# Kernel tuning notes

Measured on AMD Instinct MI355X. Metric: run time of the kernel, lower is better.

Reference implementation:

```python
import jax, jax.numpy as jnp
import numpy as np

N = 50000          # nodes per node type
E = 1_600_000      # edges per canonical etype (avg degree 32)
IN_F = 385         # BERT_EMBEDDING_DIM(384) + NUMERICAL_FEATURES(1)
H = 128            # HIDDEN_DIM
# ntype order: 0=Policy, 1=Control, 2=ComplianceRequirement, 3=Risk
# etypes (src_ntype, dst_ntype): implements, mitigates, violates, addresses, informs
ETYPES = [(0, 1), (1, 3), (3, 2), (0, 2), (2, 0)]


def setup_inputs() -> dict:
    key = jax.random.key(0)
    ks = jax.random.split(key, 12)
    inp = {}
    names = ["feat_policy", "feat_control", "feat_compliance", "feat_risk"]
    for i, n in enumerate(names):
        inp[n] = jax.random.normal(ks[i], (N, IN_F), jnp.float32)
    inp["src"] = jax.random.randint(ks[4], (5, E), 0, N, jnp.int32)
    inp["dst"] = jax.random.randint(ks[5], (5, E), 0, N, jnp.int32)
    s_in = 1.0 / np.sqrt(IN_F).astype(np.float32)
    s_h = np.sqrt(6.0 / (H + H)).astype(np.float32)  # xavier_uniform for GraphConv
    inp["Wp"] = jax.random.uniform(ks[6], (4, IN_F, H), jnp.float32, -s_in, s_in)
    inp["bp"] = jax.random.uniform(ks[7], (4, H), jnp.float32, -s_in, s_in)
    inp["Wc1"] = jax.random.uniform(ks[8], (5, H, H), jnp.float32, -s_h, s_h)
    inp["bc1"] = jnp.zeros((5, H), jnp.float32)
    inp["Wc2"] = jax.random.uniform(ks[9], (5, H, H), jnp.float32, -s_h, s_h)
    inp["bc2"] = jnp.zeros((5, H), jnp.float32)
    return inp


def _graph_conv(x, s, d, W, b):
    """DGL GraphConv(norm='both'): D_dst^{-1/2} A D_src^{-1/2} X W + b."""
    ones = jnp.ones(s.shape[0], x.dtype)
    deg_out = jnp.clip(jax.ops.segment_sum(ones, s, num_segments=N), 1.0)
    deg_in = jnp.clip(jax.ops.segment_sum(ones, d, num_segments=N), 1.0)
    xs = x * jax.lax.rsqrt(deg_out)[:, None]            # [N, H] scale by src out-deg
    agg = jax.ops.segment_sum(xs[s], d, num_segments=N)  # gather + scatter-sum [N, H]
    agg = agg * jax.lax.rsqrt(deg_in)[:, None]
    return agg @ W + b


def reference(feat_policy, feat_control, feat_compliance, feat_risk,
              src, dst, Wp, bp, Wc1, bc1, Wc2, bc2):
    feats = [feat_policy, feat_control, feat_compliance, feat_risk]
    # input projections + relu per node type
    h = [jax.nn.relu(f @ Wp[i] + bp[i]) for i, f in enumerate(feats)]

    def hetero_layer(h, Wc, bc):
        out = [jnp.zeros((N, H), h[0].dtype) for _ in range(4)]
        for k, (st, dt) in enumerate(ETYPES):  # HeteroGraphConv aggregate='sum'
            out[dt] = out[dt] + _graph_conv(h[st], src[k], dst[k], Wc[k], bc[k])
        return out

    h = [jax.nn.relu(v) for v in hetero_layer(h, Wc1, bc1)]
    h = [jax.nn.relu(v) for v in hetero_layer(h, Wc2, bc2)]
    return jnp.stack(h)  # [4, N, H] final embeddings per node type
```

## Files before the change

kernel.cpp:

```cpp
#include <hip/hip_runtime.h>
#include <hip/hip_bf16.h>

#define INF 385
#define HD 128
#define NWG 16

typedef __attribute__((ext_vector_type(8))) short short8;
typedef __attribute__((ext_vector_type(4))) float f32x4;

__device__ inline unsigned short f2b(float f) {
    __hip_bfloat16 h = __float2bfloat16(f);
    return *reinterpret_cast<unsigned short*>(&h);
}
__device__ inline float b2f(unsigned int lo16) {
    union { unsigned int u; float f; } c; c.u = lo16 << 16; return c.f;
}

__global__ __launch_bounds__(1024) void hist_kernel(
    const int* __restrict__ src_all, const int* __restrict__ dst_all,
    unsigned short* __restrict__ partial,
    unsigned short* __restrict__ rank_local,
    int E, int N)
{
    __shared__ unsigned int cnt[25000];
    int g = blockIdx.x / NWG;
    int w = blockIdx.x % NWG;
    int tid = threadIdx.x;
    int half = (N + 1) / 2;
    for (int i = tid; i < half; i += 1024) cnt[i] = 0;
    __syncthreads();

    int C = (E + NWG - 1) / NWG;
    int lo = w * C, hi = min(lo + C, E);
    if (g < 5) {
        const int* arr = dst_all + (size_t)g * E;
        for (int e = lo + tid; e < hi; e += 1024) {
            int d = __builtin_nontemporal_load(&arr[e]);
            unsigned int sh = (d & 1) * 16;
            unsigned int old = atomicAdd(&cnt[d >> 1], 1u << sh);
            rank_local[(size_t)g * E + e] = (unsigned short)((old >> sh) & 0xffffu);
        }
    } else {
        const int* arr = src_all + (size_t)(g - 5) * E;
        for (int e = lo + tid; e < hi; e += 1024) {
            int d = __builtin_nontemporal_load(&arr[e]);
            atomicAdd(&cnt[d >> 1], 1u << ((d & 1) * 16));
        }
    }
    __syncthreads();
    unsigned short* outp = partial + ((size_t)g * NWG + w) * N;
    for (int n = tid; n < N; n += 1024)
        outp[n] = (unsigned short)((cnt[n >> 1] >> ((n & 1) * 16)) & 0xffffu);
}

__global__ void reduce_kernel(unsigned short* __restrict__ partial, int* __restrict__ cnt_dst,
                              float* __restrict__ rsq_out, float* __restrict__ rsq_in, int N) {
    int i = blockIdx.x * blockDim.x + threadIdx.x;
    int stride = gridDim.x * blockDim.x;
    int tot = 10 * N;
    for (; i < tot; i += stride) {
        int g = i / N, n = i - g * N;
        unsigned short* p = partial + ((size_t)g * NWG) * N + n;
        int sum = 0;
        #pragma unroll
        for (int w = 0; w < NWG; ++w) {
            int v = p[(size_t)w * N];
            p[(size_t)w * N] = (unsigned short)sum;
            sum += v;
        }
        float r = rsqrtf((float)max(sum, 1));
        if (g < 5) { cnt_dst[i] = sum; rsq_in[i] = r; }
        else rsq_out[i - 5 * N] = r;
    }
}

__global__ __launch_bounds__(1024) void scan_kernel(const int* __restrict__ cnt_all,
                                                    int* __restrict__ off_all, int n) {
    const int* cnt = cnt_all + (size_t)blockIdx.x * n;
    int* off = off_all + (size_t)blockIdx.x * (n + 1);
    __shared__ int ssum[1024];
    int t = threadIdx.x;
    int chunk = (n + 1023) / 1024;
    int lo = t * chunk, hi = min(lo + chunk, n);
    int s = 0;
    for (int i = lo; i < hi; ++i) s += cnt[i];
    ssum[t] = s;
    __syncthreads();
    for (int d = 1; d < 1024; d <<= 1) {
        int v = (t >= d) ? ssum[t - d] : 0;
        __syncthreads();
        ssum[t] += v;
        __syncthreads();
    }
    int excl = (t == 0) ? 0 : ssum[t - 1];
    for (int i = lo; i < hi; ++i) { off[i] = excl; excl += cnt[i]; }
    if (t == 1023) off[n] = ssum[1023];
}

__global__ void permute_kernel(const int* __restrict__ src_all, const int* __restrict__ dst_all,
                               const int* __restrict__ off, const unsigned short* __restrict__ partial,
                               const unsigned short* __restrict__ rank_local,
                               unsigned short* __restrict__ sorted, int E, int N) {
    int i = blockIdx.x * blockDim.x + threadIdx.x;
    int stride = gridDim.x * blockDim.x;
    int tot = 5 * E;
    int C = (E + NWG - 1) / NWG;
    for (; i < tot; i += stride) {
        int k = i / E, e = i - k * E;
        int w = e / C;
        int d = __builtin_nontemporal_load(&dst_all[i]);
        int s = __builtin_nontemporal_load(&src_all[i]);
        int rl = __builtin_nontemporal_load(&rank_local[i]);
        int pos = off[(size_t)k * (N + 1) + d]
                + partial[((size_t)k * NWG + w) * N + d]
                + rl;
        __builtin_nontemporal_store((unsigned short)s, &sorted[(size_t)k * E + pos]);
    }
}

__global__ void convert_kernel(const float* __restrict__ f0, const float* __restrict__ f1,
                               const float* __restrict__ f2, const float* __restrict__ f3,
                               unsigned int* __restrict__ featB,
                               float* __restrict__ alast, int N) {
    int i = blockIdx.x * blockDim.x + threadIdx.x;
    int stride = gridDim.x * blockDim.x;
    int per = N * 192;
    int tot = 4 * per;
    for (int p = i; p < tot; p += stride) {
        int t = p / per, rem = p - t * per;
        int n = rem / 192, c2 = (rem - n * 192) * 2;
        const float* f = (t < 2) ? (t == 0 ? f0 : f1) : (t == 2 ? f2 : f3);
        const float* row = f + (size_t)n * INF;
        float a = row[c2], b = row[c2 + 1];
        featB[p] = ((unsigned int)f2b(b) << 16) | f2b(a);
    }
    for (int p = i; p < 4 * N; p += stride) {
        int t = p / N, n = p - t * N;
        const float* f = (t < 2) ? (t == 0 ? f0 : f1) : (t == 2 ? f2 : f3);
        alast[p] = f[(size_t)n * INF + 384];
    }
}

__global__ void prep_weights_kernel(const float* __restrict__ Wp,
                                    const float* __restrict__ Wc1, const float* __restrict__ Wc2,
                                    const float* __restrict__ bc1, const float* __restrict__ bc2,
                                    unsigned short* __restrict__ WpT,
                                    unsigned short* __restrict__ WcT,
                                    float* __restrict__ cbias) {
    int i = blockIdx.x * blockDim.x + threadIdx.x;
    int stride = gridDim.x * blockDim.x;
    const int nWp = 4 * 128 * 384;
    for (int p = i; p < nWp; p += stride) {
        int t = p / (128 * 384), rem = p % (128 * 384);
        int c = rem / 384, k = rem % 384;
        WpT[p] = f2b(Wp[(size_t)t * INF * HD + (size_t)k * HD + c]);
    }
    const int nWc = 5 * 128 * 128;
    for (int p = i; p < 2 * nWc; p += stride) {
        int layer = p / nWc, rem = p % nWc;
        int e = rem / (128 * 128), rem2 = rem % (128 * 128);
        int c = rem2 / 128, k = rem2 % 128;
        const float* W = layer ? Wc2 : Wc1;
        WcT[p] = f2b(W[(size_t)e * 128 * 128 + (size_t)k * 128 + c]);
    }
    for (int p = i; p < 2 * 4 * 128; p += stride) {
        int layer = p / 512, rem = p % 512;
        int t = rem / 128, c = rem % 128;
        const float* bc = layer ? bc2 : bc1;
        float v;
        if (t == 0) v = bc[4 * 128 + c];
        else if (t == 1) v = bc[0 * 128 + c];
        else if (t == 2) v = bc[2 * 128 + c] + bc[3 * 128 + c];
        else v = bc[1 * 128 + c];
        cbias[p] = v;
    }
}

struct GemmDesc {
    const unsigned short* A;
    const unsigned short* Bt;
    const float* bias;
    const float* rowscale;
    const float* alast;
    const float* wlast;
    unsigned short* out;
};
struct GemmBatch { GemmDesc d[5]; };

__global__ __launch_bounds__(256) void gemm_mfma_kernel(
    GemmBatch batch, int lda, int M, int K, int relu)
{
    const GemmDesc dsc = batch.d[blockIdx.y];
    const unsigned short* __restrict__ Bt = dsc.Bt;
    const unsigned short* __restrict__ A = dsc.A;

    __shared__ __align__(16) unsigned short As[64][72];
    __shared__ __align__(16) unsigned short Bs[128][72];
    const int tid = threadIdx.x;
    const int bm = blockIdx.x * 64;
    const int wid = tid >> 6, lane = tid & 63;
    const int wr = wid & 1, wc = wid >> 1;
    const int l15 = lane & 15, l4 = lane >> 4;

    f32x4 acc[2][4] = {};

    for (int k0 = 0; k0 < K; k0 += 64) {
        {
            int r = tid >> 2, q = tid & 3;
            int gm = bm + r;
            if (gm < M) {
                const uint4* g = (const uint4*)(A + (size_t)gm * lda + k0 + q * 16);
                *(uint4*)&As[r][q * 16] = g[0];
                *(uint4*)&As[r][q * 16 + 8] = g[1];
            } else {
                uint4 z = {0, 0, 0, 0};
                *(uint4*)&As[r][q * 16] = z;
                *(uint4*)&As[r][q * 16 + 8] = z;
            }
        }
        {
            int col = tid >> 1, hf = tid & 1;
            const uint4* g = (const uint4*)(Bt + (size_t)col * K + k0 + hf * 32);
            #pragma unroll
            for (int j = 0; j < 4; ++j)
                *(uint4*)&Bs[col][hf * 32 + j * 8] = g[j];
        }
        __syncthreads();
        #pragma unroll
        for (int kk = 0; kk < 2; ++kk) {
            short8 a[2], b[4];
            #pragma unroll
            for (int mi = 0; mi < 2; ++mi)
                a[mi] = *(const short8*)&As[wr * 32 + mi * 16 + l15][kk * 32 + l4 * 8];
            #pragma unroll
            for (int ni = 0; ni < 4; ++ni)
                b[ni] = *(const short8*)&Bs[wc * 64 + ni * 16 + l15][kk * 32 + l4 * 8];
            #pragma unroll
            for (int mi = 0; mi < 2; ++mi)
                #pragma unroll
                for (int ni = 0; ni < 4; ++ni)
                    acc[mi][ni] = __builtin_amdgcn_mfma_f32_16x16x32_bf16(
                        a[mi], b[ni], acc[mi][ni], 0, 0, 0);
        }
        __syncthreads();
    }

    #pragma unroll
    for (int mi = 0; mi < 2; ++mi) {
        #pragma unroll
        for (int r = 0; r < 4; ++r) {
            int grow = bm + wr * 32 + mi * 16 + l4 * 4 + r;
            if (grow >= M) continue;
            float rs = dsc.rowscale ? dsc.rowscale[grow] : 1.f;
            float al = dsc.alast ? dsc.alast[grow] : 0.f;
            #pragma unroll
            for (int ni = 0; ni < 4; ++ni) {
                int gcol = wc * 64 + ni * 16 + l15;
                float v = acc[mi][ni][r];
                if (dsc.wlast) v += al * dsc.wlast[gcol];
                if (dsc.bias) v += dsc.bias[gcol];
                v *= rs;
                if (relu) v = fmaxf(v, 0.f);
                dsc.out[(size_t)grow * HD + gcol] = f2b(v);
            }
        }
    }
}

struct GatherDesc {
    const unsigned short* msgA; const unsigned short* sortedA;
    const int* offA; const float* rsqA;
    const unsigned short* msgB; const unsigned short* sortedB;
    const int* offB; const float* rsqB;
    const float* bias; void* out;
};
struct GatherBatch { GatherDesc d[4]; };

template<int OUT_BF16>
__global__ __launch_bounds__(256) void gather_kernel(GatherBatch batch, int n)
{
    const GatherDesc d = batch.d[blockIdx.y];
    int node = blockIdx.x * 4 + (threadIdx.x >> 6);
    if (node >= n) return;
    int lane = threadIdx.x & 63;

    float ox, oy;
    {
        float ax = 0.f, ay = 0.f;
        int beg = d.offA[node], end = d.offA[node + 1];
        int e = beg;
        for (; e + 3 < end; e += 4) {
            int s0 = d.sortedA[e], s1 = d.sortedA[e + 1];
            int s2 = d.sortedA[e + 2], s3 = d.sortedA[e + 3];
            unsigned int v0 = *(const unsigned int*)(d.msgA + (size_t)s0 * HD + lane * 2);
            unsigned int v1 = *(const unsigned int*)(d.msgA + (size_t)s1 * HD + lane * 2);
            unsigned int v2 = *(const unsigned int*)(d.msgA + (size_t)s2 * HD + lane * 2);
            unsigned int v3 = *(const unsigned int*)(d.msgA + (size_t)s3 * HD + lane * 2);
            ax += b2f(v0 & 0xffffu) + b2f(v1 & 0xffffu) + b2f(v2 & 0xffffu) + b2f(v3 & 0xffffu);
            ay += b2f(v0 >> 16) + b2f(v1 >> 16) + b2f(v2 >> 16) + b2f(v3 >> 16);
        }
        for (; e < end; ++e) {
            int s0 = d.sortedA[e];
            unsigned int v0 = *(const unsigned int*)(d.msgA + (size_t)s0 * HD + lane * 2);
            ax += b2f(v0 & 0xffffu);
            ay += b2f(v0 >> 16);
        }
        float r = d.rsqA[node];
        ox = ax * r; oy = ay * r;
    }
    if (d.msgB) {
        float bx = 0.f, by = 0.f;
        int beg = d.offB[node], end = d.offB[node + 1];
        int e = beg;
        for (; e + 3 < end; e += 4) {
            int s0 = d.sortedB[e], s1 = d.sortedB[e + 1];
            int s2 = d.sortedB[e + 2], s3 = d.sortedB[e + 3];
            unsigned int v0 = *(const unsigned int*)(d.msgB + (size_t)s0 * HD + lane * 2);
            unsigned int v1 = *(const unsigned int*)(d.msgB + (size_t)s1 * HD + lane * 2);
            unsigned int v2 = *(const unsigned int*)(d.msgB + (size_t)s2 * HD + lane * 2);
            unsigned int v3 = *(const unsigned int*)(d.msgB + (size_t)s3 * HD + lane * 2);
            bx += b2f(v0 & 0xffffu) + b2f(v1 & 0xffffu) + b2f(v2 & 0xffffu) + b2f(v3 & 0xffffu);
            by += b2f(v0 >> 16) + b2f(v1 >> 16) + b2f(v2 >> 16) + b2f(v3 >> 16);
        }
        for (; e < end; ++e) {
            int s0 = d.sortedB[e];
            unsigned int v0 = *(const unsigned int*)(d.msgB + (size_t)s0 * HD + lane * 2);
            bx += b2f(v0 & 0xffffu);
            by += b2f(v0 >> 16);
        }
        float r = d.rsqB[node];
        ox += bx * r; oy += by * r;
    }
    float2 bv = *(const float2*)(d.bias + lane * 2);
    ox = fmaxf(ox + bv.x, 0.f);
    oy = fmaxf(oy + bv.y, 0.f);
    if (OUT_BF16) {
        unsigned int packed = ((unsigned int)f2b(oy) << 16) | f2b(ox);
        ((unsigned int*)d.out)[(size_t)node * (HD / 2) + lane] = packed;
    } else {
        float2 o = {ox, oy};
        ((float2*)d.out)[(size_t)node * (HD / 2) + lane] = o;
    }
}

extern "C" void kernel_launch(void* const* d_in, const int* in_sizes, int n_in,
                              void* d_out, int out_size, void* d_ws, size_t ws_size,
                              hipStream_t stream)
{
    const float* feat[4] = {(const float*)d_in[0], (const float*)d_in[1],
                            (const float*)d_in[2], (const float*)d_in[3]};
    const int* src_all = (const int*)d_in[4];
    const int* dst_all = (const int*)d_in[5];
    const float* Wp  = (const float*)d_in[6];
    const float* bp  = (const float*)d_in[7];
    const float* Wc1 = (const float*)d_in[8];
    const float* bc1 = (const float*)d_in[9];
    const float* Wc2 = (const float*)d_in[10];
    const float* bc2 = (const float*)d_in[11];

    const int N = in_sizes[0] / INF;
    const int E = in_sizes[4] / 5;

    const int st_[5] = {0, 1, 3, 0, 2};

    char* w = (char*)d_ws;
    auto take = [&](size_t bytes) { char* p = w; w += (bytes + 255) & ~(size_t)255; return p; };
    int*   cnt_dst = (int*)take(5 * (size_t)N * 4);
    float* rsq_out = (float*)take(5 * (size_t)N * 4);
    float* rsq_in  = (float*)take(5 * (size_t)N * 4);
    int*   off     = (int*)take(5 * (size_t)(N + 1) * 4);
    unsigned short* sorted = (unsigned short*)take(5 * (size_t)E * 2);
    float* alast   = (float*)take(4 * (size_t)N * 4);
    unsigned short* WpT = (unsigned short*)take(4 * 128 * 384 * 2);
    unsigned short* WcT = (unsigned short*)take(2 * 5 * 128 * 128 * 2);
    float* cbias   = (float*)take(2 * 4 * 128 * 4);
    size_t blob_sz = 4 * (size_t)N * 384 * 2;
    char* blob = (char*)take(blob_sz);
    unsigned short* partial    = (unsigned short*)blob;
    unsigned short* rank_local = (unsigned short*)(blob + 10u * NWG * (size_t)N * 2);
    unsigned short* featB      = (unsigned short*)blob;
    unsigned short* msg        = (unsigned short*)(blob + 32u * 1024 * 1024);
    unsigned short* h0 = (unsigned short*)d_out;
    unsigned short* h1 = (unsigned short*)d_out + 4 * (size_t)N * HD;

    prep_weights_kernel<<<512, 256, 0, stream>>>(Wp, Wc1, Wc2, bc1, bc2, WpT, WcT, cbias);
    hist_kernel<<<10 * NWG, 1024, 0, stream>>>(src_all, dst_all, partial, rank_local, E, N);
    reduce_kernel<<<(10 * N + 255) / 256, 256, 0, stream>>>(partial, cnt_dst, rsq_out, rsq_in, N);
    scan_kernel<<<5, 1024, 0, stream>>>(cnt_dst, off, N);
    permute_kernel<<<2048, 256, 0, stream>>>(src_all, dst_all, off, partial, rank_local,
                                             sorted, E, N);

    convert_kernel<<<2048, 256, 0, stream>>>(feat[0], feat[1], feat[2], feat[3],
                                             (unsigned int*)featB, alast, N);

    const int gblk = (N + 63) / 64;

    {
        GemmBatch pb = {};
        for (int t = 0; t < 4; ++t) {
            pb.d[t].A = featB + (size_t)t * N * 384;
            pb.d[t].Bt = WpT + (size_t)t * 128 * 384;
            pb.d[t].bias = bp + (size_t)t * HD;
            pb.d[t].rowscale = nullptr;
            pb.d[t].alast = alast + (size_t)t * N;
            pb.d[t].wlast = Wp + (size_t)t * INF * HD + 384 * HD;
            pb.d[t].out = h0 + (size_t)t * N * HD;
        }
        gemm_mfma_kernel<<<dim3(gblk, 4), 256, 0, stream>>>(pb, 384, N, 384, 1);
    }

    for (int layer = 0; layer < 2; ++layer) {
        const unsigned short* hin = layer ? h1 : h0;
        const unsigned short* WT = WcT + (size_t)layer * 5 * 128 * 128;
        const float* cb = cbias + (size_t)layer * 4 * 128;

        {
            GemmBatch cbch = {};
            for (int k = 0; k < 5; ++k) {
                cbch.d[k].A = hin + (size_t)st_[k] * N * HD;
                cbch.d[k].Bt = WT + (size_t)k * 128 * 128;
                cbch.d[k].bias = nullptr;
                cbch.d[k].rowscale = rsq_out + (size_t)k * N;
                cbch.d[k].alast = nullptr;
                cbch.d[k].wlast = nullptr;
                cbch.d[k].out = msg + (size_t)k * N * HD;
            }
            gemm_mfma_kernel<<<dim3(gblk, 5), 256, 0, stream>>>(cbch, HD, N, 128, 0);
        }

        {
            auto S = [&](int k) { return sorted + (size_t)k * E; };
            auto O = [&](int k) { return off + (size_t)k * (N + 1); };
            auto R = [&](int k) { return rsq_in + (size_t)k * N; };
            auto M_ = [&](int k) { return msg + (size_t)k * N * HD; };
            const int ksA[4] = {0, 1, 2, 4};
            const int dt [4] = {1, 3, 2, 0};
            GatherBatch gb = {};
            for (int y = 0; y < 4; ++y) {
                int k = ksA[y];
                gb.d[y].msgA = M_(k); gb.d[y].sortedA = S(k);
                gb.d[y].offA = O(k);  gb.d[y].rsqA = R(k);
                gb.d[y].msgB = nullptr; gb.d[y].sortedB = nullptr;
                gb.d[y].offB = nullptr; gb.d[y].rsqB = nullptr;
                gb.d[y].bias = cb + (size_t)dt[y] * HD;
                if (layer == 0)
                    gb.d[y].out = h1 + (size_t)dt[y] * N * HD;
                else
                    gb.d[y].out = (float*)d_out + (size_t)dt[y] * N * HD;
            }
            gb.d[2].msgB = M_(3); gb.d[2].sortedB = S(3);
            gb.d[2].offB = O(3);  gb.d[2].rsqB = R(3);
            const int gg = (N + 3) / 4;
            if (layer == 0)
                gather_kernel<1><<<dim3(gg, 4), 256, 0, stream>>>(gb, N);
            else
                gather_kernel<0><<<dim3(gg, 4), 256, 0, stream>>>(gb, N);
        }
    }
}
```

Before: 1.192 ms.

## Co-schedule histogram with feature conversion and permute with input projection

When the workspace is large enough, the feature bf16 conversion runs as extra blocks inside the histogram kernel, and the edge permutation runs as an extra grid row inside the input projection GEMM. Independent stages can then overlap on the GPU and two launches go away. This requires separate buffers for partial counts and ranks instead of aliasing them with featB. The gather loop is also unrolled to 8 edges with all index loads issued before the message loads, to raise memory-level parallelism. A fallback path keeps the old sequence when the workspace is small.

```diff
diff --git a/kernel.cpp b/kernel.cpp
--- a/kernel.cpp
+++ b/kernel.cpp
@@ -4,6 +4,7 @@
 #define INF 385
 #define HD 128
 #define NWG 16
+#define HIST_BLOCKS (10 * NWG)
 
 typedef __attribute__((ext_vector_type(8))) short short8;
 typedef __attribute__((ext_vector_type(4))) float f32x4;
@@ -16,16 +17,46 @@
     union { unsigned int u; float f; } c; c.u = lo16 << 16; return c.f;
 }
 
-__global__ __launch_bounds__(1024) void hist_kernel(
+__device__ __forceinline__ void convert_body(
+    const float* f0, const float* f1, const float* f2, const float* f3,
+    unsigned int* featB, float* alast, int N, int gid, int nthr)
+{
+    int per = N * 192;
+    int tot = 4 * per;
+    for (int p = gid; p < tot; p += nthr) {
+        int t = p / per, rem = p - t * per;
+        int n = rem / 192, c2 = (rem - n * 192) * 2;
+        const float* f = (t < 2) ? (t == 0 ? f0 : f1) : (t == 2 ? f2 : f3);
+        const float* row = f + (size_t)n * INF;
+        float a = row[c2], b = row[c2 + 1];
+        featB[p] = ((unsigned int)f2b(b) << 16) | f2b(a);
+    }
+    for (int p = gid; p < 4 * N; p += nthr) {
+        int t = p / N, n = p - t * N;
+        const float* f = (t < 2) ? (t == 0 ? f0 : f1) : (t == 2 ? f2 : f3);
+        alast[p] = f[(size_t)n * INF + 384];
+    }
+}
+
+__global__ __launch_bounds__(1024) void hist_conv_kernel(
     const int* __restrict__ src_all, const int* __restrict__ dst_all,
     unsigned short* __restrict__ partial,
     unsigned short* __restrict__ rank_local,
-    int E, int N)
+    int E, int N,
+    const float* __restrict__ f0, const float* __restrict__ f1,
+    const float* __restrict__ f2, const float* __restrict__ f3,
+    unsigned int* __restrict__ featB, float* __restrict__ alast)
 {
     __shared__ unsigned int cnt[25000];
+    int tid = threadIdx.x;
+    if (blockIdx.x >= HIST_BLOCKS) {
+        int nconv = gridDim.x - HIST_BLOCKS;
+        convert_body(f0, f1, f2, f3, featB, alast, N,
+                     (blockIdx.x - HIST_BLOCKS) * 1024 + tid, nconv * 1024);
+        return;
+    }
     int g = blockIdx.x / NWG;
     int w = blockIdx.x % NWG;
-    int tid = threadIdx.x;
     int half = (N + 1) / 2;
     for (int i = tid; i < half; i += 1024) cnt[i] = 0;
     __syncthreads();
@@ -97,15 +128,15 @@
     if (t == 1023) off[n] = ssum[1023];
 }
 
-__global__ void permute_kernel(const int* __restrict__ src_all, const int* __restrict__ dst_all,
-                               const int* __restrict__ off, const unsigned short* __restrict__ partial,
-                               const unsigned short* __restrict__ rank_local,
-                               unsigned short* __restrict__ sorted, int E, int N) {
-    int i = blockIdx.x * blockDim.x + threadIdx.x;
-    int stride = gridDim.x * blockDim.x;
+__device__ __forceinline__ void permute_body(
+    const int* __restrict__ src_all, const int* __restrict__ dst_all,
+    const int* __restrict__ off, const unsigned short* __restrict__ partial,
+    const unsigned short* __restrict__ rank_local,
+    unsigned short* __restrict__ sorted, int E, int N, int gid, int nthr)
+{
     int tot = 5 * E;
     int C = (E + NWG - 1) / NWG;
-    for (; i < tot; i += stride) {
+    for (int i = gid; i < tot; i += nthr) {
         int k = i / E, e = i - k * E;
         int w = e / C;
         int d = __builtin_nontemporal_load(&dst_all[i]);
@@ -118,27 +149,19 @@
     }
 }
 
+__global__ void permute_kernel(const int* __restrict__ src_all, const int* __restrict__ dst_all,
+                               const int* __restrict__ off, const unsigned short* __restrict__ partial,
+                               const unsigned short* __restrict__ rank_local,
+                               unsigned short* __restrict__ sorted, int E, int N) {
+    permute_body(src_all, dst_all, off, partial, rank_local, sorted, E, N,
+                 blockIdx.x * blockDim.x + threadIdx.x, gridDim.x * blockDim.x);
+}
+
 __global__ void convert_kernel(const float* __restrict__ f0, const float* __restrict__ f1,
                                const float* __restrict__ f2, const float* __restrict__ f3,
-                               unsigned int* __restrict__ featB,
-                               float* __restrict__ alast, int N) {
-    int i = blockIdx.x * blockDim.x + threadIdx.x;
-    int stride = gridDim.x * blockDim.x;
-    int per = N * 192;
-    int tot = 4 * per;
-    for (int p = i; p < tot; p += stride) {
-        int t = p / per, rem = p - t * per;
-        int n = rem / 192, c2 = (rem - n * 192) * 2;
-        const float* f = (t < 2) ? (t == 0 ? f0 : f1) : (t == 2 ? f2 : f3);
-        const float* row = f + (size_t)n * INF;
-        float a = row[c2], b = row[c2 + 1];
-        featB[p] = ((unsigned int)f2b(b) << 16) | f2b(a);
-    }
-    for (int p = i; p < 4 * N; p += stride) {
-        int t = p / N, n = p - t * N;
-        const float* f = (t < 2) ? (t == 0 ? f0 : f1) : (t == 2 ? f2 : f3);
-        alast[p] = f[(size_t)n * INF + 384];
-    }
+                               unsigned int* __restrict__ featB, float* __restrict__ alast, int N) {
+    convert_body(f0, f1, f2, f3, featB, alast, N,
+                 blockIdx.x * blockDim.x + threadIdx.x, gridDim.x * blockDim.x);
 }
 
 __global__ void prep_weights_kernel(const float* __restrict__ Wp,
@@ -187,15 +210,12 @@
 };
 struct GemmBatch { GemmDesc d[5]; };
 
-__global__ __launch_bounds__(256) void gemm_mfma_kernel(
-    GemmBatch batch, int lda, int M, int K, int relu)
-{
-    const GemmDesc dsc = batch.d[blockIdx.y];
+__device__ __forceinline__ void gemm_tile(
+    const GemmDesc& dsc, int lda, int M, int K, int relu,
+    unsigned short (*As)[72], unsigned short (*Bs)[72])
+{
     const unsigned short* __restrict__ Bt = dsc.Bt;
     const unsigned short* __restrict__ A = dsc.A;
-
-    __shared__ __align__(16) unsigned short As[64][72];
-    __shared__ __align__(16) unsigned short Bs[128][72];
     const int tid = threadIdx.x;
     const int bm = blockIdx.x * 64;
     const int wid = tid >> 6, lane = tid & 63;
@@ -267,6 +287,32 @@
     }
 }
 
+__global__ __launch_bounds__(256) void gemm_mfma_kernel(
+    GemmBatch batch, int lda, int M, int K, int relu)
+{
+    __shared__ __align__(16) unsigned short As[64][72];
+    __shared__ __align__(16) unsigned short Bs[128][72];
+    gemm_tile(batch.d[blockIdx.y], lda, M, K, relu, As, Bs);
+}
+
+__global__ __launch_bounds__(256) void permute_proj_kernel(
+    GemmBatch batch, int lda, int M, int K, int relu, int gblk,
+    const int* __restrict__ src_all, const int* __restrict__ dst_all,
+    const int* __restrict__ off, const unsigned short* __restrict__ partial,
+    const unsigned short* __restrict__ rank_local,
+    unsigned short* __restrict__ sorted, int E, int N)
+{
+    if (blockIdx.y == 4) {
+        permute_body(src_all, dst_all, off, partial, rank_local, sorted, E, N,
+                     blockIdx.x * 256 + threadIdx.x, gridDim.x * 256);
+        return;
+    }
+    if ((int)blockIdx.x >= gblk) return;
+    __shared__ __align__(16) unsigned short As[64][72];
+    __shared__ __align__(16) unsigned short Bs[128][72];
+    gemm_tile(batch.d[blockIdx.y], lda, M, K, relu, As, Bs);
+}
+
 struct GatherDesc {
     const unsigned short* msgA; const unsigned short* sortedA;
     const int* offA; const float* rsqA;
@@ -283,25 +329,30 @@
     int node = blockIdx.x * 4 + (threadIdx.x >> 6);
     if (node >= n) return;
     int lane = threadIdx.x & 63;
+    const size_t loff = (size_t)lane * 2;
 
     float ox, oy;
     {
         float ax = 0.f, ay = 0.f;
         int beg = d.offA[node], end = d.offA[node + 1];
         int e = beg;
-        for (; e + 3 < end; e += 4) {
-            int s0 = d.sortedA[e], s1 = d.sortedA[e + 1];
-            int s2 = d.sortedA[e + 2], s3 = d.sortedA[e + 3];
-            unsigned int v0 = *(const unsigned int*)(d.msgA + (size_t)s0 * HD + lane * 2);
-            unsigned int v1 = *(const unsigned int*)(d.msgA + (size_t)s1 * HD + lane * 2);
-            unsigned int v2 = *(const unsigned int*)(d.msgA + (size_t)s2 * HD + lane * 2);
-            unsigned int v3 = *(const unsigned int*)(d.msgA + (size_t)s3 * HD + lane * 2);
-            ax += b2f(v0 & 0xffffu) + b2f(v1 & 0xffffu) + b2f(v2 & 0xffffu) + b2f(v3 & 0xffffu);
-            ay += b2f(v0 >> 16) + b2f(v1 >> 16) + b2f(v2 >> 16) + b2f(v3 >> 16);
+        for (; e + 8 <= end; e += 8) {
+            int s[8];
+            unsigned int v[8];
+            #pragma unroll
+            for (int j = 0; j < 8; ++j) s[j] = d.sortedA[e + j];
+            #pragma unroll
+            for (int j = 0; j < 8; ++j)
+                v[j] = *(const unsigned int*)(d.msgA + (size_t)s[j] * HD + loff);
+            #pragma unroll
+            for (int j = 0; j < 8; ++j) {
+                ax += b2f(v[j] & 0xffffu);
+                ay += b2f(v[j] >> 16);
+            }
         }
         for (; e < end; ++e) {
             int s0 = d.sortedA[e];
-            unsigned int v0 = *(const unsigned int*)(d.msgA + (size_t)s0 * HD + lane * 2);
+            unsigned int v0 = *(const unsigned int*)(d.msgA + (size_t)s0 * HD + loff);
             ax += b2f(v0 & 0xffffu);
             ay += b2f(v0 >> 16);
         }
@@ -312,26 +363,30 @@
         float bx = 0.f, by = 0.f;
         int beg = d.offB[node], end = d.offB[node + 1];
         int e = beg;
-        for (; e + 3 < end; e += 4) {
-            int s0 = d.sortedB[e], s1 = d.sortedB[e + 1];
-            int s2 = d.sortedB[e + 2], s3 = d.sortedB[e + 3];
-            unsigned int v0 = *(const unsigned int*)(d.msgB + (size_t)s0 * HD + lane * 2);
-            unsigned int v1 = *(const unsigned int*)(d.msgB + (size_t)s1 * HD + lane * 2);
-            unsigned int v2 = *(const unsigned int*)(d.msgB + (size_t)s2 * HD + lane * 2);
-            unsigned int v3 = *(const unsigned int*)(d.msgB + (size_t)s3 * HD + lane * 2);
-            bx += b2f(v0 & 0xffffu) + b2f(v1 & 0xffffu) + b2f(v2 & 0xffffu) + b2f(v3 & 0xffffu);
-            by += b2f(v0 >> 16) + b2f(v1 >> 16) + b2f(v2 >> 16) + b2f(v3 >> 16);
+        for (; e + 8 <= end; e += 8) {
+            int s[8];
+            unsigned int v[8];
+            #pragma unroll
+            for (int j = 0; j < 8; ++j) s[j] = d.sortedB[e + j];
+            #pragma unroll
+            for (int j = 0; j < 8; ++j)
+                v[j] = *(const unsigned int*)(d.msgB + (size_t)s[j] * HD + loff);
+            #pragma unroll
+            for (int j = 0; j < 8; ++j) {
+                bx += b2f(v[j] & 0xffffu);
+                by += b2f(v[j] >> 16);
+            }
         }
         for (; e < end; ++e) {
             int s0 = d.sortedB[e];
-            unsigned int v0 = *(const unsigned int*)(d.msgB + (size_t)s0 * HD + lane * 2);
+            unsigned int v0 = *(const unsigned int*)(d.msgB + (size_t)s0 * HD + loff);
             bx += b2f(v0 & 0xffffu);
             by += b2f(v0 >> 16);
         }
         float r = d.rsqB[node];
         ox += bx * r; oy += by * r;
     }
-    float2 bv = *(const float2*)(d.bias + lane * 2);
+    float2 bv = *(const float2*)(d.bias + loff);
     ox = fmaxf(ox + bv.x, 0.f);
     oy = fmaxf(oy + bv.y, 0.f);
     if (OUT_BF16) {
@@ -374,38 +429,63 @@
     unsigned short* WpT = (unsigned short*)take(4 * 128 * 384 * 2);
     unsigned short* WcT = (unsigned short*)take(2 * 5 * 128 * 128 * 2);
     float* cbias   = (float*)take(2 * 4 * 128 * 4);
-    size_t blob_sz = 4 * (size_t)N * 384 * 2;
-    char* blob = (char*)take(blob_sz);
-    unsigned short* partial    = (unsigned short*)blob;
-    unsigned short* rank_local = (unsigned short*)(blob + 10u * NWG * (size_t)N * 2);
-    unsigned short* featB      = (unsigned short*)blob;
-    unsigned short* msg        = (unsigned short*)(blob + 32u * 1024 * 1024);
+
+    const size_t pr_bytes = 10u * NWG * (size_t)N * 2 + 5 * (size_t)E * 2;
+    const size_t blob_sz = 4 * (size_t)N * 384 * 2;
+    size_t fixed_used = (size_t)(w - (char*)d_ws);
+    bool roomy = ws_size >= fixed_used + pr_bytes + blob_sz + (1u << 20);
+
+    unsigned short *partial, *rank_local, *featB, *msg;
+    if (roomy) {
+        partial    = (unsigned short*)take(10u * NWG * (size_t)N * 2);
+        rank_local = (unsigned short*)take(5 * (size_t)E * 2);
+        char* blob = (char*)take(blob_sz);
+        featB = (unsigned short*)blob;
+        msg   = (unsigned short*)blob;
+    } else {
+        char* blob = (char*)take(blob_sz);
+        partial    = (unsigned short*)blob;
+        rank_local = (unsigned short*)(blob + 10u * NWG * (size_t)N * 2);
+        featB      = (unsigned short*)blob;
+        msg        = (unsigned short*)(blob + 32u * 1024 * 1024);
+    }
     unsigned short* h0 = (unsigned short*)d_out;
     unsigned short* h1 = (unsigned short*)d_out + 4 * (size_t)N * HD;
 
+    const int gblk = (N + 63) / 64;
+
     prep_weights_kernel<<<512, 256, 0, stream>>>(Wp, Wc1, Wc2, bc1, bc2, WpT, WcT, cbias);
-    hist_kernel<<<10 * NWG, 1024, 0, stream>>>(src_all, dst_all, partial, rank_local, E, N);
-    reduce_kernel<<<(10 * N + 255) / 256, 256, 0, stream>>>(partial, cnt_dst, rsq_out, rsq_in, N);
-    scan_kernel<<<5, 1024, 0, stream>>>(cnt_dst, off, N);
-    permute_kernel<<<2048, 256, 0, stream>>>(src_all, dst_all, off, partial, rank_local,
-                                             sorted, E, N);
-
-    convert_kernel<<<2048, 256, 0, stream>>>(feat[0], feat[1], feat[2], feat[3],
-                                             (unsigned int*)featB, alast, N);
-
-    const int gblk = (N + 63) / 64;
-
-    {
-        GemmBatch pb = {};
-        for (int t = 0; t < 4; ++t) {
-            pb.d[t].A = featB + (size_t)t * N * 384;
-            pb.d[t].Bt = WpT + (size_t)t * 128 * 384;
-            pb.d[t].bias = bp + (size_t)t * HD;
-            pb.d[t].rowscale = nullptr;
-            pb.d[t].alast = alast + (size_t)t * N;
-            pb.d[t].wlast = Wp + (size_t)t * INF * HD + 384 * HD;
-            pb.d[t].out = h0 + (size_t)t * N * HD;
-        }
+
+    GemmBatch pb = {};
+    for (int t = 0; t < 4; ++t) {
+        pb.d[t].A = featB + (size_t)t * N * 384;
+        pb.d[t].Bt = WpT + (size_t)t * 128 * 384;
+        pb.d[t].bias = bp + (size_t)t * HD;
+        pb.d[t].rowscale = nullptr;
+        pb.d[t].alast = alast + (size_t)t * N;
+        pb.d[t].wlast = Wp + (size_t)t * INF * HD + 384 * HD;
+        pb.d[t].out = h0 + (size_t)t * N * HD;
+    }
+
+    if (roomy) {
+        hist_conv_kernel<<<HIST_BLOCKS + 512, 1024, 0, stream>>>(
+            src_all, dst_all, partial, rank_local, E, N,
+            feat[0], feat[1], feat[2], feat[3], (unsigned int*)featB, alast);
+        reduce_kernel<<<(10 * N + 255) / 256, 256, 0, stream>>>(partial, cnt_dst, rsq_out, rsq_in, N);
+        scan_kernel<<<5, 1024, 0, stream>>>(cnt_dst, off, N);
+        permute_proj_kernel<<<dim3(2048, 5), 256, 0, stream>>>(
+            pb, 384, N, 384, 1, gblk,
+            src_all, dst_all, off, partial, rank_local, sorted, E, N);
+    } else {
+        hist_conv_kernel<<<HIST_BLOCKS, 1024, 0, stream>>>(
+            src_all, dst_all, partial, rank_local, E, N,
+            feat[0], feat[1], feat[2], feat[3], (unsigned int*)featB, alast);
+        reduce_kernel<<<(10 * N + 255) / 256, 256, 0, stream>>>(partial, cnt_dst, rsq_out, rsq_in, N);
+        scan_kernel<<<5, 1024, 0, stream>>>(cnt_dst, off, N);
+        permute_kernel<<<2048, 256, 0, stream>>>(src_all, dst_all, off, partial, rank_local,
+                                                 sorted, E, N);
+        convert_kernel<<<2048, 256, 0, stream>>>(feat[0], feat[1], feat[2], feat[3],
+                                                 (unsigned int*)featB, alast, N);
         gemm_mfma_kernel<<<dim3(gblk, 4), 256, 0, stream>>>(pb, 384, N, 384, 1);
     }
 
```

After: 1.146 ms. 3.8% less time.
